# Optimization experiments

Hardware: AMD Instinct MI355X
Metric: run time of the kernel (lower is better)

Reference implementation:

```python
import jax, jax.numpy as jnp
import numpy as np

B, S, D, H = 64, 1024, 256, 256


def setup_inputs() -> dict:
    key = jax.random.key(0)
    k1, k2, k3, k4, k5 = jax.random.split(key, 5)
    stdv = 1.0 / np.sqrt(H)
    x = jax.random.normal(k1, (B, S, D), dtype=jnp.float32)
    modality_lambda = jax.random.uniform(k2, (S,), dtype=jnp.float32)
    W = jax.random.uniform(k3, (D, 4 * H), minval=-stdv, maxval=stdv, dtype=jnp.float32)
    U = jax.random.uniform(k4, (H, 4 * H), minval=-stdv, maxval=stdv, dtype=jnp.float32)
    bias = jax.random.uniform(k5, (4 * H,), minval=-stdv, maxval=stdv, dtype=jnp.float32)
    return {"x": x, "modality_lambda": modality_lambda, "W": W, "U": U, "bias": bias}


def reference(x, modality_lambda, W, U, bias):
    hs = U.shape[0]
    bs = x.shape[0]
    # Precompute input projection for all timesteps in one GEMM: [S, B, 4H]
    x_proj = jnp.einsum('bsd,dg->sbg', x, W) + bias
    h0 = jnp.zeros((bs, hs), x.dtype)
    c0 = jnp.zeros((bs, hs), x.dtype)

    def step(carry, inp):
        h, c = carry
        xp, lam = inp
        gates = xp + h @ U  # [B, 4H]
        i_t = jax.nn.sigmoid(gates[:, :hs])
        f_t = jax.nn.sigmoid(gates[:, hs:2 * hs])
        g_t = jnp.tanh(gates[:, 2 * hs:3 * hs])
        o_t = jax.nn.sigmoid(gates[:, 3 * hs:])
        c = f_t * c + i_t * g_t * lam
        h = o_t * jnp.tanh(c)
        return (h, c), h

    (h_t, c_t), hidden_seq = jax.lax.scan(step, (h0, c0), (x_proj, modality_lambda))
    hidden_seq = jnp.transpose(hidden_seq, (1, 0, 2))  # [B, S, H]
    return hidden_seq, h_t, c_t
```

## Files before the change

kernel.cpp:

```cpp
#include <hip/hip_runtime.h>
#include <hip/hip_bf16.h>


#define BSH 16777216u
#define BH  16384u

typedef short short8 __attribute__((ext_vector_type(8)));
typedef float float4_ __attribute__((ext_vector_type(4)));
typedef unsigned int uint2_ __attribute__((ext_vector_type(2)));
typedef unsigned int uint4_ __attribute__((ext_vector_type(4)));

static __device__ __forceinline__ unsigned short f2bf(float f) {
    unsigned int u = __builtin_bit_cast(unsigned int, f);
    u += 0x7FFFu + ((u >> 16) & 1u);
    return (unsigned short)(u >> 16);
}
static __device__ __forceinline__ float bf2f(unsigned short h) {
    unsigned int u = ((unsigned int)h) << 16;
    return __builtin_bit_cast(float, u);
}
static __device__ __forceinline__ uint4_ pack8(const unsigned short* t) {
    uint4_ v;
    v.x = (unsigned int)t[0] | ((unsigned int)t[1] << 16);
    v.y = (unsigned int)t[2] | ((unsigned int)t[3] << 16);
    v.z = (unsigned int)t[4] | ((unsigned int)t[5] << 16);
    v.w = (unsigned int)t[6] | ((unsigned int)t[7] << 16);
    return v;
}
static __device__ __forceinline__ unsigned umin_(unsigned a, unsigned b) {
    return a < b ? a : b;
}
static __device__ __forceinline__ void gload_lds16(const void* g, void* l) {
    __builtin_amdgcn_global_load_lds(
        (const __attribute__((address_space(1))) unsigned int*)g,
        (__attribute__((address_space(3))) unsigned int*)l, 16, 0, 0);
}
static __device__ __forceinline__ void barrier_lgkm() {
    asm volatile("s_waitcnt lgkmcnt(0)" ::: "memory");
    __builtin_amdgcn_s_barrier();
    asm volatile("" ::: "memory");
}

__global__ void prep_kernel(const float* __restrict__ W, const float* __restrict__ U,
                            const float* __restrict__ bias,
                            unsigned short* __restrict__ Wbf, unsigned short* __restrict__ Ubf,
                            float* __restrict__ biasf) {
    int tid = blockIdx.x * blockDim.x + threadIdx.x;
    if (tid < 65536) {
        int idx = tid & 32767;
        const bool isU = (tid >= 32768);
        const float* src = isU ? U : W;
        unsigned short* dst = isU ? Ubf : Wbf;
        int sl = idx >> 9, kt = (idx >> 6) & 7, lane = idx & 63;
        int c = lane & 15, kgrp = lane >> 4;
        int m = sl >> 3, wv = sl & 7;
        int gatec = c >> 2, jj = c & 3;
        int ncol = gatec * 256 + 32 * m + 4 * wv + jj;
        unsigned short t8[8];
#pragma unroll
        for (int e = 0; e < 8; e++) {
            int k = kt * 32 + kgrp * 8 + e;
            float v = src[k * 1024 + ncol];
            t8[e] = f2bf(isU ? -v : v);
        }
        *(uint4_*)(dst + (size_t)idx * 8) = pack8(t8);
    } else if (tid < 66560) {
        int idx2 = tid - 65536;
        int sl = idx2 >> 4, c = idx2 & 15;
        int m = sl >> 3, wv = sl & 7, gatec = c >> 2, jj = c & 3;
        int ncol = gatec * 256 + 32 * m + 4 * wv + jj;
        biasf[idx2] = bias[ncol];
    }
}

__global__ __launch_bounds__(512, 2)
void xproj_kernel(const float* __restrict__ x, const unsigned short* __restrict__ Wbf,
                  const float* __restrict__ biasf, unsigned short* __restrict__ xp) {
    const int bx = blockIdx.x;
    const int g = bx & 3, tile = bx >> 2;
    const int s0 = tile * 4;
    const int tidx = threadIdx.x;
    const int w = tidx >> 6, lane = tidx & 63;

    __shared__ unsigned short Afrag[4][8][64][8];

    {
        int row = tidx >> 3;
        int kt = tidx & 7;
        int si = row >> 4, r = row & 15;
        int b = g * 16 + r, s = s0 + si;
        const float* px = x + ((size_t)b * 1024 + s) * 256 + kt * 32;
#pragma unroll
        for (int kg = 0; kg < 4; kg++) {
            float4_ v0 = *(const float4_*)(px + kg * 8);
            float4_ v1 = *(const float4_*)(px + kg * 8 + 4);
            unsigned short t8[8] = { f2bf(v0.x), f2bf(v0.y), f2bf(v0.z), f2bf(v0.w),
                                     f2bf(v1.x), f2bf(v1.y), f2bf(v1.z), f2bf(v1.w) };
            *(uint4_*)&Afrag[si][kt][kg * 16 + r][0] = pack8(t8);
        }
    }
    __syncthreads();

    float4_ acc[8][4];
#pragma unroll
    for (int q = 0; q < 8; q++) {
        int sl = w * 8 + q;
        float bv = biasf[sl * 16 + (lane & 15)];
#pragma unroll
        for (int si = 0; si < 4; si++) acc[q][si] = (float4_){bv, bv, bv, bv};
    }
#pragma unroll
    for (int kt = 0; kt < 8; kt++) {
        short8 a[4];
#pragma unroll
        for (int si = 0; si < 4; si++)
            a[si] = *(const short8*)&Afrag[si][kt][lane][0];
#pragma unroll
        for (int q = 0; q < 8; q++) {
            short8 bfr = *(const short8*)(Wbf + (((size_t)(w * 8 + q) * 8 + kt) * 64 + lane) * 8);
#pragma unroll
            for (int si = 0; si < 4; si++)
                acc[q][si] = __builtin_amdgcn_mfma_f32_16x16x32_bf16(a[si], bfr, acc[q][si], 0, 0, 0);
        }
    }
#pragma unroll
    for (int q = 0; q < 8; q++) {
        int sl = w * 8 + q;
        int wgx = g * 8 + (sl >> 3);
#pragma unroll
        for (int si = 0; si < 4; si++) {
            int s = s0 + si;
            unsigned int lo = (unsigned int)f2bf(acc[q][si].x) | ((unsigned int)f2bf(acc[q][si].y) << 16);
            unsigned int hi = (unsigned int)f2bf(acc[q][si].z) | ((unsigned int)f2bf(acc[q][si].w) << 16);
            uint2_ v = {lo, hi};
            *(uint2_*)(xp + ((((size_t)wgx * 1024 + s) * 8 + (sl & 7)) * 64 + lane) * 4) = v;
        }
    }
}

__global__ __launch_bounds__(576, 1)
void lstm_kernel(const unsigned short* __restrict__ Ubf,
                 const unsigned short* __restrict__ xp,
                 const float* __restrict__ lam,
                 unsigned short* __restrict__ hbuf,
                 float* __restrict__ out) {
    const int bx = blockIdx.x;
    const int g = bx & 3;
    const int m = bx >> 2;
    const int tid = threadIdx.x;
    const int w = tid >> 6, lane = tid & 63;

    __shared__ float lamLDS[1024];
    __shared__ unsigned short htmp[2][16][40];
    __shared__ unsigned short xpring[8][2048];

    for (int i = tid; i < 1024; i += 576) lamLDS[i] = lam[i];

    const int col = lane & 15;
    const int gatec = col >> 2, jj = col & 3;
    const int rr0 = (lane >> 4) * 4;
    const bool active = (gatec == 0);

    short8 u[8];
    if (w < 8) {
        int sl = m * 8 + w;
#pragma unroll
        for (int kt = 0; kt < 8; kt++)
            u[kt] = *(const short8*)(Ubf + (((size_t)sl * 8 + kt) * 64 + lane) * 8);
    }

    const size_t wgx = (size_t)(g * 8 + m);

    if (w == 8) {
        for (int s = 0; s < 6; s++) {
            const char* src = (const char*)xp + ((wgx * 1024 + s) << 12) + (size_t)lane * 16;
            char* dst = (char*)&xpring[s][0];
#pragma unroll
            for (int c2 = 0; c2 < 4; c2++)
                gload_lds16(src + c2 * 1024, dst + c2 * 1024);
        }
        asm volatile("s_waitcnt vmcnt(20)" ::: "memory");
    }
    float cst[4] = {0.f, 0.f, 0.f, 0.f};
    barrier_lgkm();

    for (int t = 0; t < 1024; t++) {
        if (w < 8) {
            unsigned long long xpd =
                *(const unsigned long long*)&xpring[t & 7][w * 256 + lane * 4];
            float4_ acc0, acc1 = (float4_){0.f, 0.f, 0.f, 0.f};
            acc0.x = bf2f((unsigned short)(xpd & 0xffff));
            acc0.y = bf2f((unsigned short)((xpd >> 16) & 0xffff));
            acc0.z = bf2f((unsigned short)((xpd >> 32) & 0xffff));
            acc0.w = bf2f((unsigned short)(xpd >> 48));

            if (t > 0) {
                const char* pb = (const char*)hbuf +
                                 (((size_t)(t - 1) * 4 + g) << 13) + (size_t)lane * 16;
                {
                    uint4_ r;
                    const char* pw = pb + w * 1024;
                    for (;;) {
                        asm volatile("global_load_dwordx4 %0, %1, off sc0 sc1\n\t"
                                     "s_waitcnt vmcnt(0)"
                                     : "=v"(r) : "v"(pw) : "memory");
                        __builtin_amdgcn_sched_barrier(0);
                        unsigned mn = umin_(umin_(r.x, r.y), umin_(r.z, r.w));
                        if (__all(mn != 0u)) break;
                    }
                }
                uint4_ r0, r1, r2, r3, r4, r5, r6, r7;
                const char* pbl = pb;
                const char* pbh = pb + 4096;
                for (;;) {
                    asm volatile(
                        "global_load_dwordx4 %0, %8, off sc0 sc1\n\t"
                        "global_load_dwordx4 %1, %8, off offset:1024 sc0 sc1\n\t"
                        "global_load_dwordx4 %2, %8, off offset:2048 sc0 sc1\n\t"
                        "global_load_dwordx4 %3, %8, off offset:3072 sc0 sc1\n\t"
                        "global_load_dwordx4 %4, %9, off sc0 sc1\n\t"
                        "global_load_dwordx4 %5, %9, off offset:1024 sc0 sc1\n\t"
                        "global_load_dwordx4 %6, %9, off offset:2048 sc0 sc1\n\t"
                        "global_load_dwordx4 %7, %9, off offset:3072 sc0 sc1\n\t"
                        "s_waitcnt vmcnt(0)"
                        : "=v"(r0), "=v"(r1), "=v"(r2), "=v"(r3),
                          "=v"(r4), "=v"(r5), "=v"(r6), "=v"(r7)
                        : "v"(pbl), "v"(pbh) : "memory");
                    __builtin_amdgcn_sched_barrier(0);
                    unsigned mn = umin_(
                        umin_(umin_(umin_(r0.x, r0.y), umin_(r0.z, r0.w)),
                              umin_(umin_(r1.x, r1.y), umin_(r1.z, r1.w))),
                        umin_(umin_(umin_(r2.x, r2.y), umin_(r2.z, r2.w)),
                              umin_(umin_(r3.x, r3.y), umin_(r3.z, r3.w))));
                    unsigned mn2 = umin_(
                        umin_(umin_(umin_(r4.x, r4.y), umin_(r4.z, r4.w)),
                              umin_(umin_(r5.x, r5.y), umin_(r5.z, r5.w))),
                        umin_(umin_(umin_(r6.x, r6.y), umin_(r6.z, r6.w)),
                              umin_(umin_(r7.x, r7.y), umin_(r7.z, r7.w))));
                    if (__all(umin_(mn, mn2) != 0u)) break;
                }
                acc0 = __builtin_amdgcn_mfma_f32_16x16x32_bf16(__builtin_bit_cast(short8, r0), u[0], acc0, 0, 0, 0);
                acc1 = __builtin_amdgcn_mfma_f32_16x16x32_bf16(__builtin_bit_cast(short8, r1), u[1], acc1, 0, 0, 0);
                acc0 = __builtin_amdgcn_mfma_f32_16x16x32_bf16(__builtin_bit_cast(short8, r2), u[2], acc0, 0, 0, 0);
                acc1 = __builtin_amdgcn_mfma_f32_16x16x32_bf16(__builtin_bit_cast(short8, r3), u[3], acc1, 0, 0, 0);
                acc0 = __builtin_amdgcn_mfma_f32_16x16x32_bf16(__builtin_bit_cast(short8, r4), u[4], acc0, 0, 0, 0);
                acc1 = __builtin_amdgcn_mfma_f32_16x16x32_bf16(__builtin_bit_cast(short8, r5), u[5], acc1, 0, 0, 0);
                acc0 = __builtin_amdgcn_mfma_f32_16x16x32_bf16(__builtin_bit_cast(short8, r6), u[6], acc0, 0, 0, 0);
                acc1 = __builtin_amdgcn_mfma_f32_16x16x32_bf16(__builtin_bit_cast(short8, r7), u[7], acc1, 0, 0, 0);
            }

            float lamt = lamLDS[t];
            float gv[4], fv[4], ggv[4], ov[4];
#pragma unroll
            for (int q = 0; q < 4; q++) {
                float xg = acc0[q] + acc1[q];
                float y = (gatec == 2) ? 2.f * xg : xg;
                float sgm = 1.f / (1.f + __expf(-y));
                gv[q] = (gatec == 2) ? 2.f * sgm - 1.f : sgm;
            }
#pragma unroll
            for (int q = 0; q < 4; q++) {
                fv[q]  = __shfl(gv[q], lane + 4, 64);
                ggv[q] = __shfl(gv[q], lane + 8, 64);
                ov[q]  = __shfl(gv[q], lane + 12, 64);
            }
            if (active) {
                float hq[4];
#pragma unroll
                for (int q = 0; q < 4; q++) {
                    float c = fv[q] * cst[q] + gv[q] * ggv[q] * lamt;
                    cst[q] = c;
                    float th = 2.f / (1.f + __expf(-2.f * c)) - 1.f;
                    hq[q] = ov[q] * th;
                }
#pragma unroll
                for (int q = 0; q < 4; q++)
                    htmp[t & 1][rr0 + q][4 * w + jj] = f2bf(-hq[q]);
                if (t == 1023) {
#pragma unroll
                    for (int q = 0; q < 4; q++) {
                        size_t b = (size_t)g * 16 + rr0 + q;
                        int j = m * 32 + 4 * w + jj;
                        out[BSH + b * 256 + j] = hq[q];
                        out[BSH + BH + b * 256 + j] = cst[q];
                    }
                }
            }
        } else if (w == 8) {
            if (t + 6 < 1024) {
                int slot = (t + 6) & 7;
                const char* src = (const char*)xp + ((wgx * 1024 + (size_t)(t + 6)) << 12)
                                  + (size_t)lane * 16;
                char* dst = (char*)&xpring[slot][0];
#pragma unroll
                for (int c2 = 0; c2 < 4; c2++)
                    gload_lds16(src + c2 * 1024, dst + c2 * 1024);
            }
            if (t > 0) {
                int r = lane >> 2, seg = lane & 3;
                uint4_ hv = *(const uint4_*)&htmp[(t - 1) & 1][r][seg * 8];
                hv.x ^= 0x80008000u; hv.y ^= 0x80008000u;
                hv.z ^= 0x80008000u; hv.w ^= 0x80008000u;
                float4_ v0 = { bf2f((unsigned short)(hv.x & 0xffff)), bf2f((unsigned short)(hv.x >> 16)),
                               bf2f((unsigned short)(hv.y & 0xffff)), bf2f((unsigned short)(hv.y >> 16)) };
                float4_ v1 = { bf2f((unsigned short)(hv.z & 0xffff)), bf2f((unsigned short)(hv.z >> 16)),
                               bf2f((unsigned short)(hv.w & 0xffff)), bf2f((unsigned short)(hv.w >> 16)) };
                float* po = out + (((size_t)(g * 16 + r)) << 18) + ((size_t)(t - 1) << 8)
                            + m * 32 + seg * 8;
                *(float4_*)po = v0;
                *(float4_*)(po + 4) = v1;
            }
            if (t == 0)            asm volatile("s_waitcnt vmcnt(20)" ::: "memory");
            else if (t == 1)       asm volatile("s_waitcnt vmcnt(22)" ::: "memory");
            else if (t + 6 < 1024) asm volatile("s_waitcnt vmcnt(24)" ::: "memory");
            else                   asm volatile("s_waitcnt vmcnt(0)"  ::: "memory");
        }
        barrier_lgkm();
        if (w == m) {
            int rr = lane & 15, kg = lane >> 4;
            uint4_ hv = *(const uint4_*)&htmp[t & 1][rr][kg * 8];
            const char* hd = (const char*)hbuf + (((size_t)t * 4 + g) << 13)
                             + m * 1024 + (size_t)lane * 16;
            asm volatile("s_waitcnt lgkmcnt(0)" ::: "memory");
            asm volatile("global_store_dwordx4 %0, %1, off sc0 sc1"
                         :: "v"(hd), "v"(hv) : "memory");
        }
    }
    if (w == 8) {
        int r = lane >> 2, seg = lane & 3;
        uint4_ hv = *(const uint4_*)&htmp[1][r][seg * 8];
        hv.x ^= 0x80008000u; hv.y ^= 0x80008000u;
        hv.z ^= 0x80008000u; hv.w ^= 0x80008000u;
        float4_ v0 = { bf2f((unsigned short)(hv.x & 0xffff)), bf2f((unsigned short)(hv.x >> 16)),
                       bf2f((unsigned short)(hv.y & 0xffff)), bf2f((unsigned short)(hv.y >> 16)) };
        float4_ v1 = { bf2f((unsigned short)(hv.z & 0xffff)), bf2f((unsigned short)(hv.z >> 16)),
                       bf2f((unsigned short)(hv.w & 0xffff)), bf2f((unsigned short)(hv.w >> 16)) };
        float* po = out + (((size_t)(g * 16 + r)) << 18) + ((size_t)1023 << 8) + m * 32 + seg * 8;
        *(float4_*)po = v0;
        *(float4_*)(po + 4) = v1;
    }
}

__global__ void ws_too_small_kernel(float* out) {
    if (threadIdx.x == 0 && blockIdx.x == 0) out[0] = -777777.0f;
}

extern "C" void kernel_launch(void* const* d_in, const int* in_sizes, int n_in,
                              void* d_out, int out_size, void* d_ws, size_t ws_size,
                              hipStream_t stream) {
    const float* x    = (const float*)d_in[0];
    const float* lam  = (const float*)d_in[1];
    const float* W    = (const float*)d_in[2];
    const float* U    = (const float*)d_in[3];
    const float* bias = (const float*)d_in[4];
    float* out = (float*)d_out;

    const size_t NEED = (size_t)162 << 20;
    if (ws_size < NEED) {
        ws_too_small_kernel<<<1, 64, 0, stream>>>(out);
        return;
    }
    char* ws = (char*)d_ws;
    unsigned short* Ubf   = (unsigned short*)(ws + (256 << 10));
    unsigned short* Wbf   = (unsigned short*)(ws + (768 << 10));
    float*          biasf = (float*)(ws + (1280 << 10));
    unsigned short* hbuf  = (unsigned short*)(ws + ((size_t)2 << 20));
    unsigned short* xp    = (unsigned short*)(ws + ((size_t)34 << 20));

    hipMemsetAsync(hbuf, 0, (size_t)32 << 20, stream);
    prep_kernel<<<260, 256, 0, stream>>>(W, U, bias, Wbf, Ubf, biasf);
    xproj_kernel<<<1024, 512, 0, stream>>>(x, Wbf, biasf, xp);
    lstm_kernel<<<32, 576, 0, stream>>>(Ubf, xp, lam, hbuf, out);
}
```

Before: 2.226 ms.

## Publish hidden state directly from gate lanes and drop pre-poll spin

```diff
diff --git a/kernel.cpp b/kernel.cpp
--- a/kernel.cpp
+++ b/kernel.cpp
@@ -27,8 +27,10 @@
     v.w = (unsigned int)t[6] | ((unsigned int)t[7] << 16);
     return v;
 }
-static __device__ __forceinline__ unsigned umin_(unsigned a, unsigned b) {
-    return a < b ? a : b;
+static __device__ __forceinline__ unsigned pkmin16(unsigned a, unsigned b) {
+    unsigned d;
+    asm("v_pk_min_u16 %0, %1, %2" : "=v"(d) : "v"(a), "v"(b));
+    return d;
 }
 static __device__ __forceinline__ void gload_lds16(const void* g, void* l) {
     __builtin_amdgcn_global_load_lds(
@@ -181,8 +183,15 @@
         }
         asm volatile("s_waitcnt vmcnt(20)" ::: "memory");
     }
+
     float cst[4] = {0.f, 0.f, 0.f, 0.f};
     barrier_lgkm();
+
+    const int u_col = 4 * w + jj;
+    char* hpub = (char*)hbuf + ((size_t)g << 13) + (size_t)m * 1024
+               + (size_t)((u_col >> 3) * 256 + rr0 * 16 + (u_col & 7) * 2);
+    const char* pbl = (const char*)hbuf + ((size_t)g << 13) + (size_t)lane * 16 - 32768;
+    const char* pbh = pbl + 4096;
 
     for (int t = 0; t < 1024; t++) {
         if (w < 8) {
@@ -195,23 +204,7 @@
             acc0.w = bf2f((unsigned short)(xpd >> 48));
 
             if (t > 0) {
-                const char* pb = (const char*)hbuf +
-                                 (((size_t)(t - 1) * 4 + g) << 13) + (size_t)lane * 16;
-                {
-                    uint4_ r;
-                    const char* pw = pb + w * 1024;
-                    for (;;) {
-                        asm volatile("global_load_dwordx4 %0, %1, off sc0 sc1\n\t"
-                                     "s_waitcnt vmcnt(0)"
-                                     : "=v"(r) : "v"(pw) : "memory");
-                        __builtin_amdgcn_sched_barrier(0);
-                        unsigned mn = umin_(umin_(r.x, r.y), umin_(r.z, r.w));
-                        if (__all(mn != 0u)) break;
-                    }
-                }
                 uint4_ r0, r1, r2, r3, r4, r5, r6, r7;
-                const char* pbl = pb;
-                const char* pbh = pb + 4096;
                 for (;;) {
                     asm volatile(
                         "global_load_dwordx4 %0, %8, off sc0 sc1\n\t"
@@ -227,17 +220,17 @@
                           "=v"(r4), "=v"(r5), "=v"(r6), "=v"(r7)
                         : "v"(pbl), "v"(pbh) : "memory");
                     __builtin_amdgcn_sched_barrier(0);
-                    unsigned mn = umin_(
-                        umin_(umin_(umin_(r0.x, r0.y), umin_(r0.z, r0.w)),
-                              umin_(umin_(r1.x, r1.y), umin_(r1.z, r1.w))),
-                        umin_(umin_(umin_(r2.x, r2.y), umin_(r2.z, r2.w)),
-                              umin_(umin_(r3.x, r3.y), umin_(r3.z, r3.w))));
-                    unsigned mn2 = umin_(
-                        umin_(umin_(umin_(r4.x, r4.y), umin_(r4.z, r4.w)),
-                              umin_(umin_(r5.x, r5.y), umin_(r5.z, r5.w))),
-                        umin_(umin_(umin_(r6.x, r6.y), umin_(r6.z, r6.w)),
-                              umin_(umin_(r7.x, r7.y), umin_(r7.z, r7.w))));
-                    if (__all(umin_(mn, mn2) != 0u)) break;
+                    unsigned q0 = pkmin16(pkmin16(r0.x, r0.y), pkmin16(r0.z, r0.w));
+                    unsigned q1 = pkmin16(pkmin16(r1.x, r1.y), pkmin16(r1.z, r1.w));
+                    unsigned q2 = pkmin16(pkmin16(r2.x, r2.y), pkmin16(r2.z, r2.w));
+                    unsigned q3 = pkmin16(pkmin16(r3.x, r3.y), pkmin16(r3.z, r3.w));
+                    unsigned q4 = pkmin16(pkmin16(r4.x, r4.y), pkmin16(r4.z, r4.w));
+                    unsigned q5 = pkmin16(pkmin16(r5.x, r5.y), pkmin16(r5.z, r5.w));
+                    unsigned q6 = pkmin16(pkmin16(r6.x, r6.y), pkmin16(r6.z, r6.w));
+                    unsigned q7 = pkmin16(pkmin16(r7.x, r7.y), pkmin16(r7.z, r7.w));
+                    unsigned mm = pkmin16(pkmin16(pkmin16(q0, q1), pkmin16(q2, q3)),
+                                          pkmin16(pkmin16(q4, q5), pkmin16(q6, q7)));
+                    if (__all(((mm & 0xffffu) != 0u) && ((mm >> 16) != 0u))) break;
                 }
                 acc0 = __builtin_amdgcn_mfma_f32_16x16x32_bf16(__builtin_bit_cast(short8, r0), u[0], acc0, 0, 0, 0);
                 acc1 = __builtin_amdgcn_mfma_f32_16x16x32_bf16(__builtin_bit_cast(short8, r1), u[1], acc1, 0, 0, 0);
@@ -266,16 +259,24 @@
             }
             if (active) {
                 float hq[4];
+                unsigned short hb[4];
 #pragma unroll
                 for (int q = 0; q < 4; q++) {
                     float c = fv[q] * cst[q] + gv[q] * ggv[q] * lamt;
                     cst[q] = c;
                     float th = 2.f / (1.f + __expf(-2.f * c)) - 1.f;
                     hq[q] = ov[q] * th;
+                    unsigned short b = f2bf(-hq[q]);
+                    if (b == 0) b = 0x8000u;
+                    hb[q] = b;
                 }
+                asm volatile("global_store_short %0, %1, off sc0 sc1"            :: "v"(hpub), "v"((unsigned)hb[0]) : "memory");
+                asm volatile("global_store_short %0, %1, off offset:16 sc0 sc1"  :: "v"(hpub), "v"((unsigned)hb[1]) : "memory");
+                asm volatile("global_store_short %0, %1, off offset:32 sc0 sc1"  :: "v"(hpub), "v"((unsigned)hb[2]) : "memory");
+                asm volatile("global_store_short %0, %1, off offset:48 sc0 sc1"  :: "v"(hpub), "v"((unsigned)hb[3]) : "memory");
 #pragma unroll
                 for (int q = 0; q < 4; q++)
-                    htmp[t & 1][rr0 + q][4 * w + jj] = f2bf(-hq[q]);
+                    htmp[t & 1][rr0 + q][4 * w + jj] = hb[q];
                 if (t == 1023) {
 #pragma unroll
                     for (int q = 0; q < 4; q++) {
@@ -316,15 +317,9 @@
             else                   asm volatile("s_waitcnt vmcnt(0)"  ::: "memory");
         }
         barrier_lgkm();
-        if (w == m) {
-            int rr = lane & 15, kg = lane >> 4;
-            uint4_ hv = *(const uint4_*)&htmp[t & 1][rr][kg * 8];
-            const char* hd = (const char*)hbuf + (((size_t)t * 4 + g) << 13)
-                             + m * 1024 + (size_t)lane * 16;
-            asm volatile("s_waitcnt lgkmcnt(0)" ::: "memory");
-            asm volatile("global_store_dwordx4 %0, %1, off sc0 sc1"
-                         :: "v"(hd), "v"(hv) : "memory");
-        }
+        hpub += 32768;
+        pbl += 32768;
+        pbh += 32768;
     }
     if (w == 8) {
         int r = lane >> 2, seg = lane & 3;
```

After: 2.287 ms. 1.03x slower.

## Split recurrent h exchange: per-wave partial publish and single-load LDS staging

Applied to the files above, without the earlier changes.

```diff
diff --git a/kernel.cpp b/kernel.cpp
--- a/kernel.cpp
+++ b/kernel.cpp
@@ -151,8 +151,9 @@
     const int w = tid >> 6, lane = tid & 63;
 
     __shared__ float lamLDS[1024];
-    __shared__ unsigned short htmp[2][16][40];
-    __shared__ unsigned short xpring[8][2048];
+    __shared__ alignas(16) unsigned short htmp[2][16][40];
+    __shared__ alignas(16) unsigned short xpring[8][2048];
+    __shared__ alignas(16) unsigned short hstage[2][8][64][8];
 
     for (int i = tid; i < 1024; i += 576) lamLDS[i] = lam[i];
 
@@ -181,10 +182,44 @@
         }
         asm volatile("s_waitcnt vmcnt(20)" ::: "memory");
     }
+
     float cst[4] = {0.f, 0.f, 0.f, 0.f};
     barrier_lgkm();
 
+    char* hpub = (char*)hbuf + ((size_t)g << 13) + (size_t)m * 1024
+               + (size_t)((w >> 1) * 256 + (w & 1) * 8) + (size_t)lane * 16;
+    const char* pb = (const char*)hbuf + ((size_t)g << 13) + (size_t)w * 1024
+                   + (size_t)lane * 16 - 32768;
+
     for (int t = 0; t < 1024; t++) {
+        if (w < 8) {
+            if (t > 0) {
+                uint4_ r;
+                for (;;) {
+                    asm volatile("global_load_dwordx4 %0, %1, off sc0 sc1\n\t"
+                                 "s_waitcnt vmcnt(0)"
+                                 : "=v"(r) : "v"(pb) : "memory");
+                    __builtin_amdgcn_sched_barrier(0);
+                    if (__all(umin_(umin_(r.x, r.y), umin_(r.z, r.w)) != 0u)) break;
+                }
+                *(uint4_*)&hstage[t & 1][w][lane][0] = r;
+            }
+        } else if (w == 8) {
+            if (t + 6 < 1024) {
+                int slot = (t + 6) & 7;
+                const char* src = (const char*)xp + ((wgx * 1024 + (size_t)(t + 6)) << 12)
+                                  + (size_t)lane * 16;
+                char* dst = (char*)&xpring[slot][0];
+#pragma unroll
+                for (int c2 = 0; c2 < 4; c2++)
+                    gload_lds16(src + c2 * 1024, dst + c2 * 1024);
+            }
+            if (t == 0)            asm volatile("s_waitcnt vmcnt(20)" ::: "memory");
+            else if (t == 1)       asm volatile("s_waitcnt vmcnt(22)" ::: "memory");
+            else if (t + 6 < 1024) asm volatile("s_waitcnt vmcnt(24)" ::: "memory");
+            else                   asm volatile("s_waitcnt vmcnt(0)"  ::: "memory");
+        }
+        barrier_lgkm();
         if (w < 8) {
             unsigned long long xpd =
                 *(const unsigned long long*)&xpring[t & 7][w * 256 + lane * 4];
@@ -195,58 +230,22 @@
             acc0.w = bf2f((unsigned short)(xpd >> 48));
 
             if (t > 0) {
-                const char* pb = (const char*)hbuf +
-                                 (((size_t)(t - 1) * 4 + g) << 13) + (size_t)lane * 16;
-                {
-                    uint4_ r;
-                    const char* pw = pb + w * 1024;
-                    for (;;) {
-                        asm volatile("global_load_dwordx4 %0, %1, off sc0 sc1\n\t"
-                                     "s_waitcnt vmcnt(0)"
-                                     : "=v"(r) : "v"(pw) : "memory");
-                        __builtin_amdgcn_sched_barrier(0);
-                        unsigned mn = umin_(umin_(r.x, r.y), umin_(r.z, r.w));
-                        if (__all(mn != 0u)) break;
-                    }
-                }
-                uint4_ r0, r1, r2, r3, r4, r5, r6, r7;
-                const char* pbl = pb;
-                const char* pbh = pb + 4096;
-                for (;;) {
-                    asm volatile(
-                        "global_load_dwordx4 %0, %8, off sc0 sc1\n\t"
-                        "global_load_dwordx4 %1, %8, off offset:1024 sc0 sc1\n\t"
-                        "global_load_dwordx4 %2, %8, off offset:2048 sc0 sc1\n\t"
-                        "global_load_dwordx4 %3, %8, off offset:3072 sc0 sc1\n\t"
-                        "global_load_dwordx4 %4, %9, off sc0 sc1\n\t"
-                        "global_load_dwordx4 %5, %9, off offset:1024 sc0 sc1\n\t"
-                        "global_load_dwordx4 %6, %9, off offset:2048 sc0 sc1\n\t"
-                        "global_load_dwordx4 %7, %9, off offset:3072 sc0 sc1\n\t"
-                        "s_waitcnt vmcnt(0)"
-                        : "=v"(r0), "=v"(r1), "=v"(r2), "=v"(r3),
-                          "=v"(r4), "=v"(r5), "=v"(r6), "=v"(r7)
-                        : "v"(pbl), "v"(pbh) : "memory");
-                    __builtin_amdgcn_sched_barrier(0);
-                    unsigned mn = umin_(
-                        umin_(umin_(umin_(r0.x, r0.y), umin_(r0.z, r0.w)),
-                              umin_(umin_(r1.x, r1.y), umin_(r1.z, r1.w))),
-                        umin_(umin_(umin_(r2.x, r2.y), umin_(r2.z, r2.w)),
-                              umin_(umin_(r3.x, r3.y), umin_(r3.z, r3.w))));
-                    unsigned mn2 = umin_(
-                        umin_(umin_(umin_(r4.x, r4.y), umin_(r4.z, r4.w)),
-                              umin_(umin_(r5.x, r5.y), umin_(r5.z, r5.w))),
-                        umin_(umin_(umin_(r6.x, r6.y), umin_(r6.z, r6.w)),
-                              umin_(umin_(r7.x, r7.y), umin_(r7.z, r7.w))));
-                    if (__all(umin_(mn, mn2) != 0u)) break;
-                }
-                acc0 = __builtin_amdgcn_mfma_f32_16x16x32_bf16(__builtin_bit_cast(short8, r0), u[0], acc0, 0, 0, 0);
-                acc1 = __builtin_amdgcn_mfma_f32_16x16x32_bf16(__builtin_bit_cast(short8, r1), u[1], acc1, 0, 0, 0);
-                acc0 = __builtin_amdgcn_mfma_f32_16x16x32_bf16(__builtin_bit_cast(short8, r2), u[2], acc0, 0, 0, 0);
-                acc1 = __builtin_amdgcn_mfma_f32_16x16x32_bf16(__builtin_bit_cast(short8, r3), u[3], acc1, 0, 0, 0);
-                acc0 = __builtin_amdgcn_mfma_f32_16x16x32_bf16(__builtin_bit_cast(short8, r4), u[4], acc0, 0, 0, 0);
-                acc1 = __builtin_amdgcn_mfma_f32_16x16x32_bf16(__builtin_bit_cast(short8, r5), u[5], acc1, 0, 0, 0);
-                acc0 = __builtin_amdgcn_mfma_f32_16x16x32_bf16(__builtin_bit_cast(short8, r6), u[6], acc0, 0, 0, 0);
-                acc1 = __builtin_amdgcn_mfma_f32_16x16x32_bf16(__builtin_bit_cast(short8, r7), u[7], acc1, 0, 0, 0);
+                short8 a0 = *(const short8*)&hstage[t & 1][0][lane][0];
+                short8 a1 = *(const short8*)&hstage[t & 1][1][lane][0];
+                short8 a2 = *(const short8*)&hstage[t & 1][2][lane][0];
+                short8 a3 = *(const short8*)&hstage[t & 1][3][lane][0];
+                short8 a4 = *(const short8*)&hstage[t & 1][4][lane][0];
+                short8 a5 = *(const short8*)&hstage[t & 1][5][lane][0];
+                short8 a6 = *(const short8*)&hstage[t & 1][6][lane][0];
+                short8 a7 = *(const short8*)&hstage[t & 1][7][lane][0];
+                acc0 = __builtin_amdgcn_mfma_f32_16x16x32_bf16(a0, u[0], acc0, 0, 0, 0);
+                acc1 = __builtin_amdgcn_mfma_f32_16x16x32_bf16(a1, u[1], acc1, 0, 0, 0);
+                acc0 = __builtin_amdgcn_mfma_f32_16x16x32_bf16(a2, u[2], acc0, 0, 0, 0);
+                acc1 = __builtin_amdgcn_mfma_f32_16x16x32_bf16(a3, u[3], acc1, 0, 0, 0);
+                acc0 = __builtin_amdgcn_mfma_f32_16x16x32_bf16(a4, u[4], acc0, 0, 0, 0);
+                acc1 = __builtin_amdgcn_mfma_f32_16x16x32_bf16(a5, u[5], acc1, 0, 0, 0);
+                acc0 = __builtin_amdgcn_mfma_f32_16x16x32_bf16(a6, u[6], acc0, 0, 0, 0);
+                acc1 = __builtin_amdgcn_mfma_f32_16x16x32_bf16(a7, u[7], acc1, 0, 0, 0);
             }
 
             float lamt = lamLDS[t];
@@ -272,10 +271,10 @@
                     cst[q] = c;
                     float th = 2.f / (1.f + __expf(-2.f * c)) - 1.f;
                     hq[q] = ov[q] * th;
+                    unsigned short b = f2bf(-hq[q]);
+                    if (b == 0) b = 0x8000u;
+                    htmp[t & 1][rr0 + q][4 * w + jj] = b;
                 }
-#pragma unroll
-                for (int q = 0; q < 4; q++)
-                    htmp[t & 1][rr0 + q][4 * w + jj] = f2bf(-hq[q]);
                 if (t == 1023) {
 #pragma unroll
                     for (int q = 0; q < 4; q++) {
@@ -286,16 +285,13 @@
                     }
                 }
             }
+            asm volatile("s_waitcnt lgkmcnt(0)" ::: "memory");
+            if (lane < 16) {
+                uint2_ chunk = *(const uint2_*)&htmp[t & 1][lane][4 * w];
+                asm volatile("global_store_dwordx2 %0, %1, off sc0 sc1"
+                             :: "v"(hpub), "v"(chunk) : "memory");
+            }
         } else if (w == 8) {
-            if (t + 6 < 1024) {
-                int slot = (t + 6) & 7;
-                const char* src = (const char*)xp + ((wgx * 1024 + (size_t)(t + 6)) << 12)
-                                  + (size_t)lane * 16;
-                char* dst = (char*)&xpring[slot][0];
-#pragma unroll
-                for (int c2 = 0; c2 < 4; c2++)
-                    gload_lds16(src + c2 * 1024, dst + c2 * 1024);
-            }
             if (t > 0) {
                 int r = lane >> 2, seg = lane & 3;
                 uint4_ hv = *(const uint4_*)&htmp[(t - 1) & 1][r][seg * 8];
@@ -310,22 +306,11 @@
                 *(float4_*)po = v0;
                 *(float4_*)(po + 4) = v1;
             }
-            if (t == 0)            asm volatile("s_waitcnt vmcnt(20)" ::: "memory");
-            else if (t == 1)       asm volatile("s_waitcnt vmcnt(22)" ::: "memory");
-            else if (t + 6 < 1024) asm volatile("s_waitcnt vmcnt(24)" ::: "memory");
-            else                   asm volatile("s_waitcnt vmcnt(0)"  ::: "memory");
-        }
-        barrier_lgkm();
-        if (w == m) {
-            int rr = lane & 15, kg = lane >> 4;
-            uint4_ hv = *(const uint4_*)&htmp[t & 1][rr][kg * 8];
-            const char* hd = (const char*)hbuf + (((size_t)t * 4 + g) << 13)
-                             + m * 1024 + (size_t)lane * 16;
-            asm volatile("s_waitcnt lgkmcnt(0)" ::: "memory");
-            asm volatile("global_store_dwordx4 %0, %1, off sc0 sc1"
-                         :: "v"(hd), "v"(hv) : "memory");
-        }
-    }
+        }
+        pb += 32768;
+        hpub += 32768;
+    }
+    barrier_lgkm();
     if (w == 8) {
         int r = lane >> 2, seg = lane & 3;
         uint4_ hv = *(const uint4_*)&htmp[1][r][seg * 8];
```

New measurement: 2.224 ms. About the same (-0.1%).
